# Kernel optimization log

Hardware: AMD Instinct MI355X
Metric: run time of the kernel (lower is better)

Reference implementation:

```python
import jax, jax.numpy as jnp
import numpy as np

B, T, D, H = 16, 81, 128, 8  # batch, ntok, d_model (= d_head), n_head


def setup_inputs() -> dict:
    key = jax.random.key(0)
    ks = jax.random.split(key, 6)
    s = 0.02
    return {
        "x": jax.random.normal(ks[0], (B, T, D), jnp.float32),
        "msk": jnp.ones((1, H, T, T), jnp.float32),
        "wqkv_w": jax.random.normal(ks[1], (H * 2 * D, D), jnp.float32) * s,
        "wqkv_b": jax.random.normal(ks[2], (H * 2 * D,), jnp.float32) * s,
        "wk_w": jax.random.normal(ks[3], (H, D), jnp.float32) * s,
        "fanout_w": jax.random.normal(ks[4], (D, D), jnp.float32) * s,
        "fanout_b": jax.random.normal(ks[5], (D,), jnp.float32) * s,
        "head_enabled": jnp.ones((H,), jnp.float32),
        "n": 0, "layer": 0, "pas": 1,
    }


def quick_gelu(x):
    return x * jax.nn.sigmoid(1.702 * x)


def reference(x, msk, wqkv_w, wqkv_b, wk_w, fanout_w, fanout_b, head_enabled, n, layer, pas):
    b, t, d = x.shape
    h = wk_w.shape[0]
    # qkv projection: per-head q and v of full width d (d_head == d_model)
    y = x @ wqkv_w.T + wqkv_b                      # [b, t, h*2*d]
    y = y.reshape(b, t, h, 2 * d)
    q, v = y[..., :d], y[..., d:]                  # [b, t, h, d] each
    # k: input gated per-head by wk.weight rows
    k = x[:, :, None, :] * wk_w[None, None, :, :]  # [b, t, h, d]
    # v gating by head-enabled flags
    v = v * head_enabled[None, None, :, None]
    # L1 attention scores: a[b,h,t,s] = -sum_d |q[b,t,h,d] - k[b,s,h,d]| / sqrt(d)
    diff = jnp.abs(q[:, :, None, :, :] - k[:, None, :, :, :])  # [b, t, s, h, d]
    a = -diff.sum(-1)                               # [b, t, s, h]
    a = jnp.transpose(a, (0, 3, 1, 2)) / jnp.sqrt(jnp.asarray(d, x.dtype))  # [b,h,t,s]
    a = jax.nn.softmax(a, axis=3) * msk
    bo = jnp.einsum('bhts,bshd->bthd', a, v)        # [b, t, h, d]
    bo = bo.sum(axis=2)                             # sum over heads -> [b, t, d]
    ap = jnp.transpose(a[0] - 1.0 + msk[0], (1, 2, 0))  # [t, s, h]
    z = quick_gelu(bo + 4.0) - 4.0
    z = z @ fanout_w.T + fanout_b
    return (x + z, ap)
```

## Files before the change

kernel.cpp:

```cpp
#include <hip/hip_runtime.h>
#include <math.h>

#define Bq 16
#define Tq 81
#define Dq 128
#define Hq 8
#define BT (Bq*Tq)
#define BTD (Bq*Tq*Dq)
#define PS 84
#define P_SZ   (Bq*Tq*Hq*PS)
#define QV_SZ  (BT*Hq*Dq)
#define P_OFF  0
#define Q_OFF  (P_OFF + P_SZ)
#define V_OFF  (Q_OFF + QV_SZ)

#define LSTR 136

typedef __attribute__((ext_vector_type(8))) short short8;
typedef __attribute__((ext_vector_type(4))) float f32x4;

__device__ __forceinline__ float l1_4(const float4 q, const float4 k) {
    return fabsf(q.x - k.x) + fabsf(q.y - k.y) + fabsf(q.z - k.z) + fabsf(q.w - k.w);
}
__device__ __forceinline__ int imin(int a, int b) { return a < b ? a : b; }
__device__ __forceinline__ unsigned short f2bf(float f) {
    unsigned u = __float_as_uint(f);
    u += 0x7fffu + ((u >> 16) & 1u);
    return (unsigned short)(u >> 16);
}
__device__ __forceinline__ float bf2f(unsigned short s) {
    return __uint_as_float((unsigned)s << 16);
}

__global__ __launch_bounds__(256) void k_qkv_mfma(
    const float* __restrict__ x, const float* __restrict__ wqkv,
    const float* __restrict__ bias, const float* __restrict__ he,
    float* __restrict__ Qo, unsigned short* __restrict__ Vb)
{
    __shared__ unsigned short xs[64 * LSTR];
    __shared__ unsigned short wsh[64 * LSTR];
    const int tid = threadIdx.x;
    const int w = tid >> 6, lane = tid & 63;
    const int ln = lane & 15, quad = lane >> 4;
    const int r0 = blockIdx.x * 64;
    const int n0 = blockIdx.y * 64;
    const int h  = blockIdx.y >> 2;
    const int isV = (blockIdx.y >> 1) & 1;
    const int c0 = (blockIdx.y & 1) * 64;

    #pragma unroll
    for (int i = 0; i < 8; ++i) {
        const int idx = tid + i * 256;
        const int r = idx >> 5, c4 = idx & 31;
        const int gr = imin(r0 + r, BT - 1);
        const float4 v = *(const float4*)(x + (size_t)gr * Dq + c4 * 4);
        ushort4 o;
        o.x = f2bf(v.x); o.y = f2bf(v.y); o.z = f2bf(v.z); o.w = f2bf(v.w);
        *(ushort4*)(&xs[r * LSTR + c4 * 4]) = o;

        const float4 vw = *(const float4*)(wqkv + (size_t)(n0 + r) * Dq + c4 * 4);
        ushort4 ow;
        ow.x = f2bf(vw.x); ow.y = f2bf(vw.y); ow.z = f2bf(vw.z); ow.w = f2bf(vw.w);
        *(ushort4*)(&wsh[r * LSTR + c4 * 4]) = ow;
    }
    __syncthreads();

    const unsigned short* xa = xs + (w * 16 + ln) * LSTR + quad * 8;
    const unsigned short* wb = wsh + ln * LSTR + quad * 8;

    f32x4 acc[4];
    #pragma unroll
    for (int i = 0; i < 4; ++i) acc[i] = (f32x4){0.f, 0.f, 0.f, 0.f};

    #pragma unroll
    for (int kb = 0; kb < Dq; kb += 32) {
        const short8 af = *(const short8*)(xa + kb);
        #pragma unroll
        for (int nt = 0; nt < 4; ++nt) {
            const short8 bf = *(const short8*)(wb + nt * 16 * LSTR + kb);
            acc[nt] = __builtin_amdgcn_mfma_f32_16x16x32_bf16(af, bf, acc[nt], 0, 0, 0);
        }
    }

    const float scale = isV ? he[h] : 1.0f;
    const int gm0 = r0 + w * 16 + quad * 4;
    #pragma unroll
    for (int nt = 0; nt < 4; ++nt) {
        const float bn = bias[n0 + nt * 16 + ln];
        #pragma unroll
        for (int r = 0; r < 4; ++r) {
            const int gm = gm0 + r;
            if (gm < BT) {
                const int bb = gm / 81, tt = gm - bb * 81;
                const size_t o =
                    (((size_t)bb * Hq + h) * Tq + tt) * Dq + c0 + nt * 16 + ln;
                const float val = (acc[nt][r] + bn) * scale;
                if (isV) Vb[o] = f2bf(val);
                else     Qo[o] = val;
            }
        }
    }
}

__global__ __launch_bounds__(512) void k_attn_out(
    const float* __restrict__ x, const float* __restrict__ Q,
    const float* __restrict__ wk, const float* __restrict__ msk,
    const unsigned short* __restrict__ Vb, const float* __restrict__ fw,
    const float* __restrict__ fb, float* __restrict__ out)
{
    __shared__ float xl[Tq * Dq];
    __shared__ float Pl[Hq][6][PS];
    __shared__ float bo_part[Hq][6][Dq];
    __shared__ float zs[6][Dq];

    const int tid = threadIdx.x;
    const int t0 = blockIdx.x * 6, b = blockIdx.y;
    const int w = tid >> 6, lane = tid & 63;

    for (int idx = tid; idx < Tq * 32; idx += 512) {
        const int r = idx >> 5, g = idx & 31;
        const float4 v = *(const float4*)(x + (size_t)(b * Tq + r) * Dq + g * 4);
        *(float4*)(&xl[r * Dq + ((g ^ (r & 7)) << 2)]) = v;
    }
    __syncthreads();

    const int s0 = lane;
    const bool has1 = (lane < Tq - 64);
    const int s1 = 64 + lane;
    const int s1c = has1 ? s1 : (Tq - 1);
    int ttv[6];
    const float* qrow[6];
    #pragma unroll
    for (int i = 0; i < 6; ++i) {
        ttv[i] = imin(t0 + i, Tq - 1);
        qrow[i] = Q + (((size_t)b * Hq + w) * Tq + ttv[i]) * Dq;
    }
    const float* wkb = wk + (size_t)w * Dq;

    float acc0[6], acc1[6];
    #pragma unroll
    for (int i = 0; i < 6; ++i) { acc0[i] = 0.f; acc1[i] = 0.f; }

    #pragma unroll 2
    for (int g = 0; g < 32; ++g) {
        const float4 wv = *(const float4*)(wkb + g * 4);
        float4 k0 = *(const float4*)(&xl[s0 * Dq + ((g ^ (s0 & 7)) << 2)]);
        float4 k1 = *(const float4*)(&xl[s1c * Dq + ((g ^ (s1c & 7)) << 2)]);
        k0.x *= wv.x; k0.y *= wv.y; k0.z *= wv.z; k0.w *= wv.w;
        k1.x *= wv.x; k1.y *= wv.y; k1.z *= wv.z; k1.w *= wv.w;
        #pragma unroll
        for (int i = 0; i < 6; ++i) {
            const float4 qv = *(const float4*)(qrow[i] + g * 4);
            acc0[i] += l1_4(qv, k0);
            acc1[i] += l1_4(qv, k1);
        }
    }

    {
        const float ns = -0.08838834764831845f;
        #pragma unroll
        for (int i = 0; i < 6; ++i) {
            const float v0 = acc0[i] * ns;
            const float v1 = has1 ? acc1[i] * ns : -1e30f;
            float m = fmaxf(v0, v1);
            #pragma unroll
            for (int off = 32; off > 0; off >>= 1)
                m = fmaxf(m, __shfl_xor(m, off));
            const float e0 = __expf(v0 - m);
            const float e1 = has1 ? __expf(v1 - m) : 0.f;
            float ssum = e0 + e1;
            #pragma unroll
            for (int off = 32; off > 0; off >>= 1)
                ssum += __shfl_xor(ssum, off);
            const float rinv = 1.0f / ssum;
            const float* mrow = msk + ((size_t)w * Tq + ttv[i]) * Tq;
            const bool tvalid = (t0 + i) < Tq;
            const float mv0 = mrow[s0];
            const float p0 = e0 * rinv * mv0;
            Pl[w][i][s0] = p0;
            if (b == 0 && tvalid)
                out[BTD + ((size_t)(t0 + i) * Tq + s0) * Hq + w] = p0 - 1.0f + mv0;
            if (has1) {
                const float mv1 = mrow[s1];
                const float p1 = e1 * rinv * mv1;
                Pl[w][i][s1] = p1;
                if (b == 0 && tvalid)
                    out[BTD + ((size_t)(t0 + i) * Tq + s1) * Hq + w] = p1 - 1.0f + mv1;
            }
        }
    }
    __syncthreads();

    {
        const int d0 = lane * 2;
        float2 acc[6];
        #pragma unroll
        for (int i = 0; i < 6; ++i) acc[i] = make_float2(0.f, 0.f);
        const unsigned short* vp = Vb + (((size_t)b * Hq + w) * Tq) * Dq + d0;
        for (int s4 = 0; s4 < 20; ++s4) {
            float4 p[6];
            #pragma unroll
            for (int t = 0; t < 6; ++t)
                p[t] = *(const float4*)(&Pl[w][t][s4 * 4]);
            #pragma unroll
            for (int ss = 0; ss < 4; ++ss) {
                const int s = s4 * 4 + ss;
                const ushort2 uv = *(const ushort2*)(vp + (size_t)s * Dq);
                const float vx = bf2f(uv.x), vy = bf2f(uv.y);
                #pragma unroll
                for (int t = 0; t < 6; ++t) {
                    const float pv = ((const float*)&p[t])[ss];
                    acc[t].x = fmaf(pv, vx, acc[t].x);
                    acc[t].y = fmaf(pv, vy, acc[t].y);
                }
            }
        }
        {
            const ushort2 uv = *(const ushort2*)(vp + (size_t)80 * Dq);
            const float vx = bf2f(uv.x), vy = bf2f(uv.y);
            #pragma unroll
            for (int t = 0; t < 6; ++t) {
                const float pv = Pl[w][t][80];
                acc[t].x = fmaf(pv, vx, acc[t].x);
                acc[t].y = fmaf(pv, vy, acc[t].y);
            }
        }
        #pragma unroll
        for (int t = 0; t < 6; ++t) {
            bo_part[w][t][d0]     = acc[t].x;
            bo_part[w][t][d0 + 1] = acc[t].y;
        }
    }
    __syncthreads();

    for (int idx = tid; idx < 768; idx += 512) {
        const int t = idx >> 7, d = idx & 127;
        float bo = 0.f;
        #pragma unroll
        for (int ww = 0; ww < 8; ++ww) bo += bo_part[ww][t][d];
        const float tt2 = bo + 4.0f;
        const float sg = 1.0f / (1.0f + __expf(-1.702f * tt2));
        zs[t][d] = tt2 * sg - 4.0f;
    }
    __syncthreads();

    {
        const int n = tid & 127, tg = tid >> 7;
        const bool two = (tg < 2);
        const int tB = two ? tg + 4 : tg;
        const float* fwr = fw + (size_t)n * Dq;
        const float fbn = fb[n];
        float a0 = 0.f, a1 = 0.f;
        #pragma unroll 8
        for (int k4 = 0; k4 < 32; ++k4) {
            const float4 w4 = *(const float4*)(fwr + k4 * 4);
            const float4 z0 = *(const float4*)(&zs[tg][k4 * 4]);
            const float4 z1 = *(const float4*)(&zs[tB][k4 * 4]);
            a0 += z0.x * w4.x + z0.y * w4.y + z0.z * w4.z + z0.w * w4.w;
            a1 += z1.x * w4.x + z1.y * w4.y + z1.z * w4.z + z1.w * w4.w;
        }
        const int t1 = t0 + tg;
        if (t1 < Tq) {
            const size_t o = ((size_t)b * Tq + t1) * Dq + n;
            out[o] = x[o] + a0 + fbn;
        }
        const int t2 = t0 + tg + 4;
        if (two && t2 < Tq) {
            const size_t o = ((size_t)b * Tq + t2) * Dq + n;
            out[o] = x[o] + a1 + fbn;
        }
    }
}

extern "C" void kernel_launch(void* const* d_in, const int* in_sizes, int n_in,
                              void* d_out, int out_size, void* d_ws, size_t ws_size,
                              hipStream_t stream) {
    const float* x        = (const float*)d_in[0];
    const float* msk      = (const float*)d_in[1];
    const float* wqkv_w   = (const float*)d_in[2];
    const float* wqkv_b   = (const float*)d_in[3];
    const float* wk_w     = (const float*)d_in[4];
    const float* fanout_w = (const float*)d_in[5];
    const float* fanout_b = (const float*)d_in[6];
    const float* he       = (const float*)d_in[7];
    float* out = (float*)d_out;
    float* ws  = (float*)d_ws;

    float* Q  = ws + Q_OFF;
    unsigned short* Vb = (unsigned short*)(ws + V_OFF);

    k_qkv_mfma<<<dim3(21, 32), 256, 0, stream>>>(x, wqkv_w, wqkv_b, he, Q, Vb);
    k_attn_out<<<dim3(14, 16), 512, 0, stream>>>(x, Q, wk_w, msk, Vb,
                                                 fanout_w, fanout_b, out);
}
```

Measured before the change: 120.5 us.

## Halve query-chunk size, stage Q and wk in LDS, rebalance tail keys

```diff
diff --git a/kernel.cpp b/kernel.cpp
--- a/kernel.cpp
+++ b/kernel.cpp
@@ -15,6 +15,9 @@
 #define V_OFF  (Q_OFF + QV_SZ)
 
 #define LSTR 136
+
+#define TCH 3
+#define NCH 27
 
 typedef __attribute__((ext_vector_type(8))) short short8;
 typedef __attribute__((ext_vector_type(4))) float f32x4;
@@ -108,13 +111,16 @@
     const unsigned short* __restrict__ Vb, const float* __restrict__ fw,
     const float* __restrict__ fb, float* __restrict__ out)
 {
-    __shared__ float xl[Tq * Dq];
-    __shared__ float Pl[Hq][6][PS];
-    __shared__ float bo_part[Hq][6][Dq];
-    __shared__ float zs[6][Dq];
+    __shared__ float smem[14464];
+    __shared__ float Pl[Hq][TCH][PS];
+    float* const xl  = smem;
+    float* const Ql  = smem + 10368;
+    float* const wkl = smem + 13440;
+    float* const bo  = smem;
+    float* const zs  = smem + 4096;
 
     const int tid = threadIdx.x;
-    const int t0 = blockIdx.x * 6, b = blockIdx.y;
+    const int t0 = blockIdx.x * TCH, b = blockIdx.y;
     const int w = tid >> 6, lane = tid & 63;
 
     for (int idx = tid; idx < Tq * 32; idx += 512) {
@@ -122,46 +128,64 @@
         const float4 v = *(const float4*)(x + (size_t)(b * Tq + r) * Dq + g * 4);
         *(float4*)(&xl[r * Dq + ((g ^ (r & 7)) << 2)]) = v;
     }
-    __syncthreads();
-
-    const int s0 = lane;
-    const bool has1 = (lane < Tq - 64);
-    const int s1 = 64 + lane;
-    const int s1c = has1 ? s1 : (Tq - 1);
-    int ttv[6];
-    const float* qrow[6];
-    #pragma unroll
-    for (int i = 0; i < 6; ++i) {
-        ttv[i] = imin(t0 + i, Tq - 1);
-        qrow[i] = Q + (((size_t)b * Hq + w) * Tq + ttv[i]) * Dq;
-    }
-    const float* wkb = wk + (size_t)w * Dq;
-
-    float acc0[6], acc1[6];
-    #pragma unroll
-    for (int i = 0; i < 6; ++i) { acc0[i] = 0.f; acc1[i] = 0.f; }
-
-    #pragma unroll 2
-    for (int g = 0; g < 32; ++g) {
-        const float4 wv = *(const float4*)(wkb + g * 4);
-        float4 k0 = *(const float4*)(&xl[s0 * Dq + ((g ^ (s0 & 7)) << 2)]);
-        float4 k1 = *(const float4*)(&xl[s1c * Dq + ((g ^ (s1c & 7)) << 2)]);
-        k0.x *= wv.x; k0.y *= wv.y; k0.z *= wv.z; k0.w *= wv.w;
-        k1.x *= wv.x; k1.y *= wv.y; k1.z *= wv.z; k1.w *= wv.w;
-        #pragma unroll
-        for (int i = 0; i < 6; ++i) {
-            const float4 qv = *(const float4*)(qrow[i] + g * 4);
-            acc0[i] += l1_4(qv, k0);
-            acc1[i] += l1_4(qv, k1);
-        }
-    }
-
-    {
-        const float ns = -0.08838834764831845f;
-        #pragma unroll
-        for (int i = 0; i < 6; ++i) {
+    for (int idx = tid; idx < Hq * TCH * 32; idx += 512) {
+        const int row = idx >> 5, g = idx & 31;
+        const int h = row / TCH, i = row - h * TCH;
+        const float4 v =
+            *(const float4*)(Q + (((size_t)b * Hq + h) * Tq + t0 + i) * Dq + g * 4);
+        *(float4*)(&Ql[row * Dq + g * 4]) = v;
+    }
+    if (tid < 256) {
+        const float4 v = *(const float4*)(wk + tid * 4);
+        *(float4*)(&wkl[tid * 4]) = v;
+    }
+    __syncthreads();
+
+    const float* wkw = wkl + w * Dq;
+    const float* qb  = Ql + w * TCH * Dq;
+    float acc0[TCH];
+    #pragma unroll
+    for (int i = 0; i < TCH; ++i) acc0[i] = 0.f;
+    {
+        const int s = lane;
+        #pragma unroll 2
+        for (int g = 0; g < 32; ++g) {
+            const float4 wv = *(const float4*)(wkw + g * 4);
+            float4 k0 = *(const float4*)(&xl[s * Dq + ((g ^ (s & 7)) << 2)]);
+            k0.x *= wv.x; k0.y *= wv.y; k0.z *= wv.z; k0.w *= wv.w;
+            #pragma unroll
+            for (int i = 0; i < TCH; ++i) {
+                const float4 qv = *(const float4*)(qb + i * Dq + g * 4);
+                acc0[i] += l1_4(qv, k0);
+            }
+        }
+    }
+    const float ns = -0.08838834764831845f;
+    {
+        if (lane < TCH * 17) {
+            const int tt = lane / 17, j = lane - tt * 17;
+            const int s = 64 + j;
+            float a = 0.f;
+            #pragma unroll 2
+            for (int g = 0; g < 32; ++g) {
+                const float4 wv = *(const float4*)(wkw + g * 4);
+                float4 kv = *(const float4*)(&xl[s * Dq + ((g ^ (s & 7)) << 2)]);
+                kv.x *= wv.x; kv.y *= wv.y; kv.z *= wv.z; kv.w *= wv.w;
+                const float4 qv = *(const float4*)(qb + tt * Dq + g * 4);
+                a += l1_4(qv, kv);
+            }
+            Pl[w][tt][s] = a * ns;
+        }
+    }
+    __syncthreads();
+
+    {
+        const bool has1 = (lane < Tq - 64);
+        const int s1 = 64 + lane;
+        #pragma unroll
+        for (int i = 0; i < TCH; ++i) {
             const float v0 = acc0[i] * ns;
-            const float v1 = has1 ? acc1[i] * ns : -1e30f;
+            const float v1 = has1 ? Pl[w][i][s1] : -1e30f;
             float m = fmaxf(v0, v1);
             #pragma unroll
             for (int off = 32; off > 0; off >>= 1)
@@ -173,18 +197,17 @@
             for (int off = 32; off > 0; off >>= 1)
                 ssum += __shfl_xor(ssum, off);
             const float rinv = 1.0f / ssum;
-            const float* mrow = msk + ((size_t)w * Tq + ttv[i]) * Tq;
-            const bool tvalid = (t0 + i) < Tq;
-            const float mv0 = mrow[s0];
+            const float* mrow = msk + ((size_t)w * Tq + (t0 + i)) * Tq;
+            const float mv0 = mrow[lane];
             const float p0 = e0 * rinv * mv0;
-            Pl[w][i][s0] = p0;
-            if (b == 0 && tvalid)
-                out[BTD + ((size_t)(t0 + i) * Tq + s0) * Hq + w] = p0 - 1.0f + mv0;
+            Pl[w][i][lane] = p0;
+            if (b == 0)
+                out[BTD + ((size_t)(t0 + i) * Tq + lane) * Hq + w] = p0 - 1.0f + mv0;
             if (has1) {
                 const float mv1 = mrow[s1];
                 const float p1 = e1 * rinv * mv1;
                 Pl[w][i][s1] = p1;
-                if (b == 0 && tvalid)
+                if (b == 0)
                     out[BTD + ((size_t)(t0 + i) * Tq + s1) * Hq + w] = p1 - 1.0f + mv1;
             }
         }
@@ -193,14 +216,14 @@
 
     {
         const int d0 = lane * 2;
-        float2 acc[6];
-        #pragma unroll
-        for (int i = 0; i < 6; ++i) acc[i] = make_float2(0.f, 0.f);
+        float2 acc[TCH];
+        #pragma unroll
+        for (int i = 0; i < TCH; ++i) acc[i] = make_float2(0.f, 0.f);
         const unsigned short* vp = Vb + (((size_t)b * Hq + w) * Tq) * Dq + d0;
         for (int s4 = 0; s4 < 20; ++s4) {
-            float4 p[6];
-            #pragma unroll
-            for (int t = 0; t < 6; ++t)
+            float4 p[TCH];
+            #pragma unroll
+            for (int t = 0; t < TCH; ++t)
                 p[t] = *(const float4*)(&Pl[w][t][s4 * 4]);
             #pragma unroll
             for (int ss = 0; ss < 4; ++ss) {
@@ -208,7 +231,7 @@
                 const ushort2 uv = *(const ushort2*)(vp + (size_t)s * Dq);
                 const float vx = bf2f(uv.x), vy = bf2f(uv.y);
                 #pragma unroll
-                for (int t = 0; t < 6; ++t) {
+                for (int t = 0; t < TCH; ++t) {
                     const float pv = ((const float*)&p[t])[ss];
                     acc[t].x = fmaf(pv, vx, acc[t].x);
                     acc[t].y = fmaf(pv, vy, acc[t].y);
@@ -219,55 +242,44 @@
             const ushort2 uv = *(const ushort2*)(vp + (size_t)80 * Dq);
             const float vx = bf2f(uv.x), vy = bf2f(uv.y);
             #pragma unroll
-            for (int t = 0; t < 6; ++t) {
+            for (int t = 0; t < TCH; ++t) {
                 const float pv = Pl[w][t][80];
                 acc[t].x = fmaf(pv, vx, acc[t].x);
                 acc[t].y = fmaf(pv, vy, acc[t].y);
             }
         }
         #pragma unroll
-        for (int t = 0; t < 6; ++t) {
-            bo_part[w][t][d0]     = acc[t].x;
-            bo_part[w][t][d0 + 1] = acc[t].y;
-        }
-    }
-    __syncthreads();
-
-    for (int idx = tid; idx < 768; idx += 512) {
+        for (int t = 0; t < TCH; ++t) {
+            bo[(w * TCH + t) * Dq + d0]     = acc[t].x;
+            bo[(w * TCH + t) * Dq + d0 + 1] = acc[t].y;
+        }
+    }
+    __syncthreads();
+
+    for (int idx = tid; idx < TCH * Dq; idx += 512) {
         const int t = idx >> 7, d = idx & 127;
-        float bo = 0.f;
-        #pragma unroll
-        for (int ww = 0; ww < 8; ++ww) bo += bo_part[ww][t][d];
-        const float tt2 = bo + 4.0f;
+        float s = 0.f;
+        #pragma unroll
+        for (int ww = 0; ww < 8; ++ww) s += bo[(ww * TCH + t) * Dq + d];
+        const float tt2 = s + 4.0f;
         const float sg = 1.0f / (1.0f + __expf(-1.702f * tt2));
-        zs[t][d] = tt2 * sg - 4.0f;
+        zs[t * Dq + d] = tt2 * sg - 4.0f;
     }
     __syncthreads();
 
     {
         const int n = tid & 127, tg = tid >> 7;
-        const bool two = (tg < 2);
-        const int tB = two ? tg + 4 : tg;
-        const float* fwr = fw + (size_t)n * Dq;
-        const float fbn = fb[n];
-        float a0 = 0.f, a1 = 0.f;
-        #pragma unroll 8
-        for (int k4 = 0; k4 < 32; ++k4) {
-            const float4 w4 = *(const float4*)(fwr + k4 * 4);
-            const float4 z0 = *(const float4*)(&zs[tg][k4 * 4]);
-            const float4 z1 = *(const float4*)(&zs[tB][k4 * 4]);
-            a0 += z0.x * w4.x + z0.y * w4.y + z0.z * w4.z + z0.w * w4.w;
-            a1 += z1.x * w4.x + z1.y * w4.y + z1.z * w4.z + z1.w * w4.w;
-        }
-        const int t1 = t0 + tg;
-        if (t1 < Tq) {
-            const size_t o = ((size_t)b * Tq + t1) * Dq + n;
-            out[o] = x[o] + a0 + fbn;
-        }
-        const int t2 = t0 + tg + 4;
-        if (two && t2 < Tq) {
-            const size_t o = ((size_t)b * Tq + t2) * Dq + n;
-            out[o] = x[o] + a1 + fbn;
+        if (tg < TCH) {
+            const float* fwr = fw + (size_t)n * Dq;
+            float a0 = 0.f;
+            #pragma unroll 8
+            for (int k4 = 0; k4 < 32; ++k4) {
+                const float4 w4 = *(const float4*)(fwr + k4 * 4);
+                const float4 z0 = *(const float4*)(&zs[tg * Dq + k4 * 4]);
+                a0 += z0.x * w4.x + z0.y * w4.y + z0.z * w4.z + z0.w * w4.w;
+            }
+            const size_t o = ((size_t)b * Tq + t0 + tg) * Dq + n;
+            out[o] = x[o] + a0 + fb[n];
         }
     }
 }
@@ -290,6 +302,6 @@
     unsigned short* Vb = (unsigned short*)(ws + V_OFF);
 
     k_qkv_mfma<<<dim3(21, 32), 256, 0, stream>>>(x, wqkv_w, wqkv_b, he, Q, Vb);
-    k_attn_out<<<dim3(14, 16), 512, 0, stream>>>(x, Q, wk_w, msk, Vb,
-                                                 fanout_w, fanout_b, out);
-}
+    k_attn_out<<<dim3(NCH, 16), 512, 0, stream>>>(x, Q, wk_w, msk, Vb,
+                                                  fanout_w, fanout_b, out);
+}
```

Result: faster. 114.8 us (-4.7%).
